# Performance work log

Measured on AMD Instinct MI355X. Metric: run time of the kernel, lower is better.

## Reference

```python
import jax, jax.numpy as jnp
import numpy as np

NUM_HEADS = 16
HEAD_DIM = 64
HIDDEN = NUM_HEADS * HEAD_DIM  # 1024
MAX_POS = 1024


def setup_inputs() -> dict:
    key = jax.random.key(0)
    ks = jax.random.split(key, 6)
    B, L, H = 8, 1024, HIDDEN
    hidden_states = jax.random.normal(ks[0], (B, L, H), dtype=jnp.float32)
    attention_mask = jnp.zeros((B, 1, 1, L), dtype=jnp.float32)
    scale = 0.02  # keep pre-softmax logits in a sane range
    Wq = jax.random.normal(ks[1], (H, H), dtype=jnp.float32) * scale
    Wk = jax.random.normal(ks[2], (H, H), dtype=jnp.float32) * scale
    Wv = jax.random.normal(ks[3], (H, H), dtype=jnp.float32) * scale
    bq = jnp.zeros((H,), dtype=jnp.float32)
    bk = jnp.zeros((H,), dtype=jnp.float32)
    bv = jnp.zeros((H,), dtype=jnp.float32)
    dist_emb = jax.random.normal(ks[4], (2 * MAX_POS - 1, HEAD_DIM), dtype=jnp.float32) * scale
    return {"hidden_states": hidden_states, "attention_mask": attention_mask,
            "Wq": Wq, "bq": bq, "Wk": Wk, "bk": bk, "Wv": Wv, "bv": bv,
            "dist_emb": dist_emb}


def _split_heads(x):
    # [B, L, H] -> [B, nH, L, hd]
    B, L, _ = x.shape
    return x.reshape(B, L, NUM_HEADS, HEAD_DIM).transpose(0, 2, 1, 3)


def reference(hidden_states, attention_mask, Wq, bq, Wk, bk, Wv, bv, dist_emb):
    B, L, H = hidden_states.shape
    q = _split_heads(hidden_states @ Wq.T + bq)  # [B,h,L,d]
    k = _split_heads(hidden_states @ Wk.T + bk)
    v = _split_heads(hidden_states @ Wv.T + bv)

    scores = jnp.einsum("bhld,bhrd->bhlr", q, k)

    # relative_key_query positional bias
    pos_l = jnp.arange(L)[:, None]
    pos_r = jnp.arange(L)[None, :]
    dist_idx = pos_l - pos_r + MAX_POS - 1          # [L, L], in [0, 2*MAX_POS-2]
    pos_emb = dist_emb[dist_idx]                    # [L, L, d]
    scores = scores + jnp.einsum("bhld,lrd->bhlr", q, pos_emb)
    scores = scores + jnp.einsum("bhrd,lrd->bhlr", k, pos_emb)

    scores = scores / jnp.sqrt(jnp.float32(HEAD_DIM))
    scores = scores + attention_mask                # additive mask broadcast [B,1,1,L]
    probs = jax.nn.softmax(scores, axis=-1)         # dropout = identity (eval)
    ctx = jnp.einsum("bhlr,bhrd->bhld", probs, v)
    ctx = ctx.transpose(0, 2, 1, 3).reshape(B, L, H)
    return ctx
```

## Files before the change

### kernel.cpp

```cpp
#include <hip/hip_runtime.h>
#include <stdint.h>

typedef short s16x8 __attribute__((ext_vector_type(8)));
typedef float f32x4 __attribute__((ext_vector_type(4)));

#define MFMA16(a, b, c) __builtin_amdgcn_mfma_f32_16x16x32_bf16((a), (b), (c), 0, 0, 0)

__device__ __forceinline__ ushort f2b(float f) {
  union { float f; uint32_t u; } x; x.f = f;
  uint32_t r = x.u + 0x7fffu + ((x.u >> 16) & 1u);
  return (ushort)(r >> 16);
}
__device__ __forceinline__ float b2f(ushort s) {
  union { uint32_t u; float f; } x; x.u = ((uint32_t)s) << 16;
  return x.f;
}
__device__ __forceinline__ uint32_t pack2t(float a, float b) {
  return __builtin_amdgcn_perm(__float_as_uint(b), __float_as_uint(a), 0x07060302u);
}
__device__ __forceinline__ uint32_t cvtpk(float a, float b) {
  uint32_t r;
  asm("v_cvt_pk_bf16_f32 %0, %1, %2" : "=v"(r) : "v"(a), "v"(b));
  return r;
}

__device__ __forceinline__ void barrier_vm() {
  asm volatile("s_waitcnt vmcnt(0)" ::: "memory");
  __builtin_amdgcn_s_barrier();
}
__device__ __forceinline__ void barrier_lgkm() {
  asm volatile("s_waitcnt lgkmcnt(0)" ::: "memory");
  __builtin_amdgcn_s_barrier();
}

__global__ __launch_bounds__(256) void cast_all(
    const float* __restrict__ hidden, const float* __restrict__ wq,
    const float* __restrict__ wk, const float* __restrict__ wv,
    const float* __restrict__ dist,
    ushort* __restrict__ hb, ushort* __restrict__ wb, ushort* __restrict__ eb) {
  int blk = blockIdx.x;
  const float* src; ushort* dst; int n;
  if (blk < 8192)      { src = hidden; dst = hb; n = 8388608; }
  else if (blk < 9216) { src = wq; dst = wb;               n = 1048576; blk -= 8192; }
  else if (blk < 10240){ src = wk; dst = wb + 1048576;     n = 1048576; blk -= 9216; }
  else if (blk < 11264){ src = wv; dst = wb + 2097152;     n = 1048576; blk -= 10240; }
  else                 { src = dist; dst = eb;             n = 131008;  blk -= 11264; }
  int i = (blk * 256 + threadIdx.x) * 4;
  if (i + 4 <= n) {
    float4 v = *(const float4*)(src + i);
    ushort4 o; o.x = f2b(v.x); o.y = f2b(v.y); o.z = f2b(v.z); o.w = f2b(v.w);
    *(ushort4*)(dst + i) = o;
  }
}

__device__ __forceinline__ void gload16(const void* g, void* l) {
  __builtin_amdgcn_global_load_lds((const __attribute__((address_space(1))) void*)g,
                                   (__attribute__((address_space(3))) void*)l, 16, 0, 0);
}

__global__ __launch_bounds__(256) void qkv_gemm(
    const ushort* __restrict__ hb, const ushort* __restrict__ wb,
    const float* __restrict__ bq, const float* __restrict__ bk, const float* __restrict__ bv,
    ushort* __restrict__ qb, ushort* __restrict__ kb, ushort* __restrict__ vt) {
  __shared__ ushort As[2][4096];
  __shared__ ushort Bs[2][4096];
  const int tid = threadIdx.x;
  const int w = tid >> 6, lane = tid & 63, quad = lane >> 4, l16 = lane & 15;

  const int wg = blockIdx.x;
  const int swz = (wg & 7) * 192 + (wg >> 3);
  const int by = swz / 24;
  const int bx = swz % 24;
  const int m0 = by * 128, n0 = bx * 128;

  const int srow = w * 32 + (lane >> 2);
  const int scol = (lane & 3) * 8;
  const ushort* ga = hb + (size_t)(m0 + srow) * 1024 + scol;
  const ushort* gw = wb + (size_t)(n0 + srow) * 1024 + scol;

  f32x4 acc[4][4];
#pragma unroll
  for (int mt = 0; mt < 4; ++mt)
#pragma unroll
    for (int nt = 0; nt < 4; ++nt) acc[mt][nt] = (f32x4){0.f, 0.f, 0.f, 0.f};

  const int wm = (w >> 1) * 64, wn = (w & 1) * 64;

#define STAGE(C, K0)                                          \
  gload16(ga + (K0), As[C] + w * 1024);                       \
  gload16(ga + (K0) + 16 * 1024, As[C] + w * 1024 + 512);     \
  gload16(gw + (K0), Bs[C] + w * 1024);                       \
  gload16(gw + (K0) + 16 * 1024, Bs[C] + w * 1024 + 512);

#define COMPUTE(C)                                                           \
  {                                                                          \
    s16x8 af[4], bfr[4];                                                     \
    _Pragma("unroll")                                                        \
    for (int mt = 0; mt < 4; ++mt)                                           \
      af[mt] = *(const s16x8*)(As[C] + (wm + 16 * mt + l16) * 32 + quad * 8);\
    _Pragma("unroll")                                                        \
    for (int nt = 0; nt < 4; ++nt)                                           \
      bfr[nt] = *(const s16x8*)(Bs[C] + (wn + 16 * nt + l16) * 32 + quad * 8);\
    _Pragma("unroll")                                                        \
    for (int mt = 0; mt < 4; ++mt)                                           \
      _Pragma("unroll")                                                      \
      for (int nt = 0; nt < 4; ++nt)                                         \
        acc[mt][nt] = MFMA16(af[mt], bfr[nt], acc[mt][nt]);                  \
  }

  STAGE(0, 0)
#pragma unroll 1
  for (int t2 = 0; t2 < 16; ++t2) {
    barrier_vm();
    STAGE(1, t2 * 64 + 32)
    COMPUTE(0)
    barrier_vm();
    if (t2 < 15) { STAGE(0, t2 * 64 + 64) }
    COMPUTE(1)
  }
#undef STAGE
#undef COMPUTE

  const int mat = n0 >> 10;
  const int b = m0 >> 10;
  if (mat < 2) {
    ushort* outp = (mat == 0) ? qb : kb;
    const float* bias = (mat == 0) ? bq : bk;
#pragma unroll
    for (int mt = 0; mt < 4; ++mt) {
      int mbase = m0 + wm + 16 * mt + 4 * quad;
#pragma unroll
      for (int nt = 0; nt < 4; ++nt) {
        int n = n0 + wn + 16 * nt + l16;
        int o = n & 1023; int hh = o >> 6; int d = o & 63;
        float bsv = bias[o];
#pragma unroll
        for (int reg = 0; reg < 4; ++reg) {
          int l = (mbase + reg) & 1023;
          outp[(((size_t)(b * 16 + hh)) * 1024 + l) * 64 + d] = f2b(acc[mt][nt][reg] + bsv);
        }
      }
    }
  } else {
#pragma unroll
    for (int mt = 0; mt < 4; ++mt) {
      int mbase = m0 + wm + 16 * mt + 4 * quad;
      int lb = mbase & 1023;
#pragma unroll
      for (int nt = 0; nt < 4; ++nt) {
        int n = n0 + wn + 16 * nt + l16;
        int o = n & 1023; int hh = o >> 6; int d = o & 63;
        float bsv = bv[o];
        uint2 pk;
        pk.x = cvtpk(acc[mt][nt][0] + bsv, acc[mt][nt][1] + bsv);
        pk.y = cvtpk(acc[mt][nt][2] + bsv, acc[mt][nt][3] + bsv);
        *(uint2*)(vt + (((size_t)(b * 16 + hh)) * 64 + d) * 1024 + lb) = pk;
      }
    }
  }
}

#define KR  0
#define VR  8192
#define ER  16384
#define SER 28672
#define PR  35072

__global__ __launch_bounds__(256, 2) void attn_kernel(
    const ushort* __restrict__ qb, const ushort* __restrict__ kb,
    const ushort* __restrict__ vt, const ushort* __restrict__ eb,
    const float* __restrict__ mask, float* __restrict__ out, int bh0) {
  __shared__ __align__(16) ushort sm[39168];
  const int tid = threadIdx.x;
  const int w = tid >> 6, lane = tid & 63, quad = lane >> 4, l16 = lane & 15;
  const int bh = blockIdx.y + bh0, b = bh >> 4, h = bh & 15;
  const int l0 = blockIdx.x * 64;

  const int srow = lane >> 3;
  const int colb = ((lane & 7) ^ srow) * 8;
  const int row0 = w * 8 + srow;

  const ushort* kp = kb + ((size_t)bh * 1024 + row0) * 64 + colb;
  const ushort* vp = vt + ((size_t)bh * 64 + row0) * 1024 + colb;
  const float* maskp = mask + b * 1024 + l16;

  const int p0 = blockIdx.x % 3;

  {
    const ushort* qp = qb + ((size_t)bh * 1024 + l0 + row0) * 64 + colb;
    gload16(qp,         sm + PR + w * 512);
    gload16(qp + 2048,  sm + PR + 2048 + w * 512);
    gload16(kp,         sm + KR + w * 512);
    gload16(kp + 2048,  sm + KR + 2048 + w * 512);
    gload16(vp,         sm + VR + w * 512);
    gload16(vp + 32768, sm + VR + 2048 + w * 512);
    const int t0i = l0 + 960;
#pragma unroll
    for (int c2 = 0; c2 < 4; ++c2) {
      int jb = w * 8 + 32 * c2;
      int seg = p0 + (jb >> 6); if (seg >= 3) seg -= 3;
      int t = t0i + jb + srow; if (t > 2046) t = 2046;
      gload16(eb + (size_t)t * 64 + colb, sm + ER + seg * 4096 + (jb & 63) * 64);
    }
  }

  const int lm7 = l16 & 7;
  const int swzq = (quad ^ lm7) * 8;
  int offR0[4], offR1[4];
#pragma unroll
  for (int nt = 0; nt < 4; ++nt) {
    offR0[nt] = (16 * nt + l16) * 64 + swzq;
    offR1[nt] = offR0[nt] ^ 32;
  }
  const int offW0 = (w * 16 + l16) * 64 + swzq;
  const int offW1 = offW0 ^ 32;
  const int offPW0 = PR + offW0, offPW1 = PR + offW1;
  const int offWK0 = ((3 - w) * 16 + l16) * 64 + swzq;
  const int offWK1 = offWK0 ^ 32;
  int eoffA[5]; bool selA[5];
#pragma unroll
  for (int i = 0; i < 5; ++i) {
    int ba = w + i;
    eoffA[i] = ((ba & 3) * 16 + l16) * 64 + swzq;  selA[i] = (ba & 4) != 0;
  }
  int offSW[5];
#pragma unroll
  for (int i = 0; i < 5; ++i)
    offSW[i] = SER + (3 - w) * 1600 + (16 * i + l16) * 20 + 4 * quad;
  const int bbF = SER + (w * 16 + 4 * quad + 15 - l16) * 20 + l16;
  int addrP[4][4];
#pragma unroll
  for (int nt = 0; nt < 4; ++nt)
#pragma unroll
    for (int reg = 0; reg < 4; ++reg)
      addrP[nt][reg] = PR + (w * 16 + 4 * quad + reg) * 64
                     + (((2 * nt + (l16 >> 3)) ^ ((4 * quad + reg) & 7)) * 8) + lm7;
  int bidx[4]; bool bcnd[4];
#pragma unroll
  for (int r = 0; r < 4; ++r) {
    bidx[r] = (quad * 16 + ((4 * quad + r + 15 - l16) & 15)) * 4;
    bcnd[r] = (4 * quad + r) > l16;
  }

  barrier_vm();

  const s16x8 aq0 = *(const s16x8*)(sm + offPW0);
  const s16x8 aq1 = *(const s16x8*)(sm + offPW1);

  float rsum[4];
  f32x4 o_acc[4];
#pragma unroll
  for (int r = 0; r < 4; ++r) rsum[r] = 0.f;
#pragma unroll
  for (int nt = 0; nt < 4; ++nt) o_acc[nt] = (f32x4){0.f, 0.f, 0.f, 0.f};
  const f32x4 ZACC = {0.f, 0.f, 0.f, 0.f};

  const float LOG2E = 1.44269504088896f;
  const float SC = 0.125f * LOG2E;

  int s0 = p0;

#define ATTN_ITER(P)                                                               \
  {                                                                                \
    const int it = 2 * ith + (P);                                                  \
    const int r0 = it * 64;                                                        \
    if (it > 0) barrier_vm();     \
          \
    {                                                                              \
      const int rn = (r0 + 64) & 1023;                                             \
      gload16(kp + rn * 64,        sm + KR + 4096 * (1 - (P)) + w * 512);          \
      gload16(kp + rn * 64 + 2048, sm + KR + 4096 * (1 - (P)) + 2048 + w * 512);   \
      gload16(vp + rn,             sm + VR + 4096 * (1 - (P)) + w * 512);          \
      gload16(vp + rn + 32768,     sm + VR + 4096 * (1 - (P)) + 2048 + w * 512);   \
      int pnew = s0 + 2; if (pnew >= 3) pnew -= 3;                                 \
      const int tb = l0 + 960 - r0 - 64;                                           \
      _Pragma("unroll")                                                            \
      for (int c2 = 0; c2 < 2; ++c2) {                                             \
        int o = w * 8 + 32 * c2;                                                   \
        int t = tb + o + srow; t = t < 0 ? 0 : (t > 2046 ? 2046 : t);              \
        gload16(eb + (size_t)t * 64 + colb, sm + ER + pnew * 4096 + o * 64);       \
      }                                                                            \
    }                                                                              \
    float mkv[4];                                                                  \
    _Pragma("unroll")                                                              \
    for (int nt = 0; nt < 4; ++nt) mkv[nt] = maskp[r0 + 16 * nt] * LOG2E;          \
    const int sA4 = s0 * 4096;                                                     \
    int sBi = s0 + 1; if (sBi >= 3) sBi -= 3;                                      \
    const int sB4 = sBi * 4096;                                                    \
    const ushort* KbP = sm + KR + 4096 * (P);                                      \
                                              \
    __builtin_amdgcn_s_setprio(1);                                                 \
    f32x4 zv[4];                                                                   \
    _Pragma("unroll")                                                              \
    for (int nt = 0; nt < 4; ++nt) {                                               \
      s16x8 bk0 = *(const s16x8*)(KbP + offR0[nt]);                                \
      s16x8 bk1 = *(const s16x8*)(KbP + offR1[nt]);                                \
      f32x4 z = MFMA16(aq0, bk0, ZACC);                                            \
      zv[nt] = MFMA16(aq1, bk1, z);                                                \
    }                                                                              \
     \
    const s16x8 ak0 = *(const s16x8*)(KbP + offWK0);                               \
    const s16x8 ak1 = *(const s16x8*)(KbP + offWK1);                               \
    f32x4 d1[5];                                                                   \
    _Pragma("unroll")                                                              \
    for (int i = 0; i < 5; ++i) {                                                  \
      int ea = (selA[i] ? sB4 : sA4) + eoffA[i];                                   \
      s16x8 be0 = *(const s16x8*)(sm + ER + ea);                                   \
      s16x8 be1 = *(const s16x8*)(sm + ER + (ea ^ 32));                            \
      f32x4 z = MFMA16(aq0, be0, ZACC);                                            \
      d1[i] = MFMA16(aq1, be1, z);                                                 \
      f32x4 y = MFMA16(ak0, be0, ZACC);                                            \
      y = MFMA16(ak1, be1, y);                                                     \
      uint2 pk; pk.x = pack2t(y[0], y[1]); pk.y = pack2t(y[2], y[3]);              \
      *(uint2*)(sm + offSW[i]) = pk;                                               \
    }                                                                              \
    __builtin_amdgcn_s_setprio(0);                                                 \
                                  \
    _Pragma("unroll")                                                              \
    for (int r = 0; r < 4; ++r) {                                                  \
      float bp[5];                                                                 \
      _Pragma("unroll")                                                            \
      for (int i = 0; i < 5; ++i)                                                  \
        bp[i] = __int_as_float(                                                    \
            __builtin_amdgcn_ds_bpermute(bidx[r], __float_as_int(d1[i][r])));      \
      _Pragma("unroll")                                                            \
      for (int nt = 0; nt < 4; ++nt)                                               \
        zv[nt][r] += bcnd[r] ? bp[4 - nt] : bp[3 - nt];                            \
    }                                                                              \
    barrier_lgkm();                   \
                    \
    _Pragma("unroll")                                                              \
    for (int nt = 0; nt < 4; ++nt) {                                               \
      _Pragma("unroll")                                                            \
      for (int reg = 0; reg < 4; ++reg) {                                          \
        float z2 = (zv[nt][reg] + b2f(sm[bbF + nt * 1600 + reg * 20])) * SC        \
                 + mkv[nt];                                                        \
        float pe = exp2f(z2);                                                      \
        zv[nt][reg] = pe;                                                          \
        rsum[reg] += pe;                                                           \
      }                                                                            \
    }                                                                              \
               \
    _Pragma("unroll")                                                              \
    for (int nt = 0; nt < 4; ++nt) {                                               \
      uint32_t u01 = cvtpk(zv[nt][0], zv[nt][1]);                                  \
      uint32_t u23 = cvtpk(zv[nt][2], zv[nt][3]);                                  \
      sm[addrP[nt][0]] = (ushort)u01;                                              \
      sm[addrP[nt][1]] = (ushort)(u01 >> 16);                                      \
      sm[addrP[nt][2]] = (ushort)u23;                                              \
      sm[addrP[nt][3]] = (ushort)(u23 >> 16);                                      \
    }                                                                              \
       \
    __builtin_amdgcn_s_setprio(1);                                                 \
    {                                                                              \
      const ushort* VbP = sm + VR + 4096 * (P);                                    \
      const s16x8 ap0 = *(const s16x8*)(sm + offPW0);                              \
      _Pragma("unroll")                                                            \
      for (int nt = 0; nt < 4; ++nt) {                                             \
        s16x8 bv0 = *(const s16x8*)(VbP + offR0[nt]);                              \
        o_acc[nt] = MFMA16(ap0, bv0, o_acc[nt]);                                   \
      }                                                                            \
      const s16x8 ap1 = *(const s16x8*)(sm + offPW1);                              \
      _Pragma("unroll")                                                            \
      for (int nt = 0; nt < 4; ++nt) {                                             \
        s16x8 bv1 = *(const s16x8*)(VbP + offR1[nt]);                              \
        o_acc[nt] = MFMA16(ap1, bv1, o_acc[nt]);                                   \
      }                                                                            \
    }                                                                              \
    __builtin_amdgcn_s_setprio(0);                                                 \
    s0 = (s0 == 0) ? 2 : s0 - 1;                   \
  }

#pragma unroll 1
  for (int ith = 0; ith < 8; ++ith) {
    ATTN_ITER(0)
    ATTN_ITER(1)
  }
#undef ATTN_ITER

#pragma unroll
  for (int off = 1; off < 16; off <<= 1)
#pragma unroll
    for (int reg = 0; reg < 4; ++reg)
      rsum[reg] += __shfl_xor(rsum[reg], off);

#pragma unroll
  for (int nt = 0; nt < 4; ++nt)
#pragma unroll
    for (int reg = 0; reg < 4; ++reg) {
      int l = l0 + w * 16 + 4 * quad + reg;
      int d = 16 * nt + l16;
      out[((size_t)(b * 1024 + l)) * 1024 + h * 64 + d] = o_acc[nt][reg] / rsum[reg];
    }
}

extern "C" void kernel_launch(void* const* d_in, const int* in_sizes, int n_in,
                              void* d_out, int out_size, void* d_ws, size_t ws_size,
                              hipStream_t stream) {
  const float* hidden = (const float*)d_in[0];
  const float* mask   = (const float*)d_in[1];
  const float* Wq     = (const float*)d_in[2];
  const float* bq     = (const float*)d_in[3];
  const float* Wk     = (const float*)d_in[4];
  const float* bk     = (const float*)d_in[5];
  const float* Wv     = (const float*)d_in[6];
  const float* bv     = (const float*)d_in[7];
  const float* dist   = (const float*)d_in[8];
  float* out = (float*)d_out;

  ushort* ws = (ushort*)d_ws;
  ushort* qb = ws;
  ushort* kb = ws + 8388608;
  ushort* vt = ws + 16777216;
  ushort* hb = ws + 25165824;
  ushort* wb = ws + 33554432;
  ushort* eb = ws + 36700160;

  cast_all<<<11392, 256, 0, stream>>>(hidden, Wq, Wk, Wv, dist, hb, wb, eb);
  qkv_gemm<<<1536, 256, 0, stream>>>(hb, wb, bq, bk, bv, qb, kb, vt);
  attn_kernel<<<dim3(16, 64), 256, 0, stream>>>(qb, kb, vt, eb, mask, out, 0);
  attn_kernel<<<dim3(16, 64), 256, 0, stream>>>(qb, kb, vt, eb, mask, out, 64);
}
```

Measured before the change: 372.1 us.

## Enlarge QKV GEMM tile to 256x128 and merge attention launches

The QKV projection GEMM now computes 256x128 output tiles per block, with each wave handling 128 rows in two halves that reuse the same B fragments. The grid is halved and the swizzle adjusted, and the barrier now also waits on LDS counters. The two half-size attention launches are merged into one 128-head-batch launch to cut launch overhead and tail effects. The larger tile doubles the accumulator registers and A-tile LDS, which may reduce occupancy despite the launch-bounds hint of 3.

```diff
diff --git a/kernel.cpp b/kernel.cpp
--- a/kernel.cpp
+++ b/kernel.cpp
@@ -26,6 +26,10 @@
 
 __device__ __forceinline__ void barrier_vm() {
   asm volatile("s_waitcnt vmcnt(0)" ::: "memory");
+  __builtin_amdgcn_s_barrier();
+}
+__device__ __forceinline__ void barrier_vm_lgkm() {
+  asm volatile("s_waitcnt vmcnt(0) lgkmcnt(0)" ::: "memory");
   __builtin_amdgcn_s_barrier();
 }
 __device__ __forceinline__ void barrier_lgkm() {
@@ -58,63 +62,70 @@
                                    (__attribute__((address_space(3))) void*)l, 16, 0, 0);
 }
 
-__global__ __launch_bounds__(256) void qkv_gemm(
+__global__ __launch_bounds__(256, 3) void qkv_gemm(
     const ushort* __restrict__ hb, const ushort* __restrict__ wb,
     const float* __restrict__ bq, const float* __restrict__ bk, const float* __restrict__ bv,
     ushort* __restrict__ qb, ushort* __restrict__ kb, ushort* __restrict__ vt) {
-  __shared__ ushort As[2][4096];
+  __shared__ ushort As[2][8192];
   __shared__ ushort Bs[2][4096];
   const int tid = threadIdx.x;
   const int w = tid >> 6, lane = tid & 63, quad = lane >> 4, l16 = lane & 15;
 
   const int wg = blockIdx.x;
-  const int swz = (wg & 7) * 192 + (wg >> 3);
+  const int swz = (wg & 7) * 96 + (wg >> 3);
   const int by = swz / 24;
   const int bx = swz % 24;
-  const int m0 = by * 128, n0 = bx * 128;
-
-  const int srow = w * 32 + (lane >> 2);
-  const int scol = (lane & 3) * 8;
-  const ushort* ga = hb + (size_t)(m0 + srow) * 1024 + scol;
-  const ushort* gw = wb + (size_t)(n0 + srow) * 1024 + scol;
-
-  f32x4 acc[4][4];
-#pragma unroll
-  for (int mt = 0; mt < 4; ++mt)
+  const int m0 = by * 256, n0 = bx * 128;
+
+  const int arow = lane >> 2;
+  const int acol = (lane & 3) * 8;
+  const ushort* ga = hb + (size_t)(m0 + arow) * 1024 + acol;
+  const ushort* gw = wb + (size_t)(n0 + arow) * 1024 + acol;
+
+  f32x4 acc[8][4];
+#pragma unroll
+  for (int mt = 0; mt < 8; ++mt)
 #pragma unroll
     for (int nt = 0; nt < 4; ++nt) acc[mt][nt] = (f32x4){0.f, 0.f, 0.f, 0.f};
 
-  const int wm = (w >> 1) * 64, wn = (w & 1) * 64;
-
-#define STAGE(C, K0)                                          \
-  gload16(ga + (K0), As[C] + w * 1024);                       \
-  gload16(ga + (K0) + 16 * 1024, As[C] + w * 1024 + 512);     \
-  gload16(gw + (K0), Bs[C] + w * 1024);                       \
-  gload16(gw + (K0) + 16 * 1024, Bs[C] + w * 1024 + 512);
-
-#define COMPUTE(C)                                                           \
-  {                                                                          \
-    s16x8 af[4], bfr[4];                                                     \
-    _Pragma("unroll")                                                        \
-    for (int mt = 0; mt < 4; ++mt)                                           \
-      af[mt] = *(const s16x8*)(As[C] + (wm + 16 * mt + l16) * 32 + quad * 8);\
-    _Pragma("unroll")                                                        \
-    for (int nt = 0; nt < 4; ++nt)                                           \
+  const int wm = (w >> 1) * 128, wn = (w & 1) * 64;
+
+#define STAGE(C, K0)                                                      \
+  gload16(ga + (K0) + (size_t)((w)      * 16) * 1024, As[C] + (w)      * 512); \
+  gload16(ga + (K0) + (size_t)((w + 4)  * 16) * 1024, As[C] + (w + 4)  * 512); \
+  gload16(ga + (K0) + (size_t)((w + 8)  * 16) * 1024, As[C] + (w + 8)  * 512); \
+  gload16(ga + (K0) + (size_t)((w + 12) * 16) * 1024, As[C] + (w + 12) * 512); \
+  gload16(gw + (K0) + (size_t)((w)      * 16) * 1024, Bs[C] + (w)      * 512); \
+  gload16(gw + (K0) + (size_t)((w + 4)  * 16) * 1024, Bs[C] + (w + 4)  * 512);
+
+#define COMPUTE(C)                                                            \
+  {                                                                           \
+    s16x8 bfr[4];                                                             \
+    _Pragma("unroll")                                                         \
+    for (int nt = 0; nt < 4; ++nt)                                            \
       bfr[nt] = *(const s16x8*)(Bs[C] + (wn + 16 * nt + l16) * 32 + quad * 8);\
-    _Pragma("unroll")                                                        \
-    for (int mt = 0; mt < 4; ++mt)                                           \
-      _Pragma("unroll")                                                      \
-      for (int nt = 0; nt < 4; ++nt)                                         \
-        acc[mt][nt] = MFMA16(af[mt], bfr[nt], acc[mt][nt]);                  \
+    _Pragma("unroll")                                                         \
+    for (int half = 0; half < 2; ++half) {                                    \
+      s16x8 af[4];                                                            \
+      _Pragma("unroll")                                                       \
+      for (int mt = 0; mt < 4; ++mt)                                          \
+        af[mt] = *(const s16x8*)(As[C] +                                      \
+                    (wm + 64 * half + 16 * mt + l16) * 32 + quad * 8);        \
+      _Pragma("unroll")                                                       \
+      for (int mt = 0; mt < 4; ++mt)                                          \
+        _Pragma("unroll")                                                     \
+        for (int nt = 0; nt < 4; ++nt)                                        \
+          acc[half * 4 + mt][nt] = MFMA16(af[mt], bfr[nt], acc[half * 4 + mt][nt]); \
+    }                                                                         \
   }
 
   STAGE(0, 0)
 #pragma unroll 1
   for (int t2 = 0; t2 < 16; ++t2) {
-    barrier_vm();
+    barrier_vm_lgkm();
     STAGE(1, t2 * 64 + 32)
     COMPUTE(0)
-    barrier_vm();
+    barrier_vm_lgkm();
     if (t2 < 15) { STAGE(0, t2 * 64 + 64) }
     COMPUTE(1)
   }
@@ -127,7 +138,7 @@
     ushort* outp = (mat == 0) ? qb : kb;
     const float* bias = (mat == 0) ? bq : bk;
 #pragma unroll
-    for (int mt = 0; mt < 4; ++mt) {
+    for (int mt = 0; mt < 8; ++mt) {
       int mbase = m0 + wm + 16 * mt + 4 * quad;
 #pragma unroll
       for (int nt = 0; nt < 4; ++nt) {
@@ -143,7 +154,7 @@
     }
   } else {
 #pragma unroll
-    for (int mt = 0; mt < 4; ++mt) {
+    for (int mt = 0; mt < 8; ++mt) {
       int mbase = m0 + wm + 16 * mt + 4 * quad;
       int lb = mbase & 1023;
 #pragma unroll
@@ -169,11 +180,11 @@
 __global__ __launch_bounds__(256, 2) void attn_kernel(
     const ushort* __restrict__ qb, const ushort* __restrict__ kb,
     const ushort* __restrict__ vt, const ushort* __restrict__ eb,
-    const float* __restrict__ mask, float* __restrict__ out, int bh0) {
+    const float* __restrict__ mask, float* __restrict__ out) {
   __shared__ __align__(16) ushort sm[39168];
   const int tid = threadIdx.x;
   const int w = tid >> 6, lane = tid & 63, quad = lane >> 4, l16 = lane & 15;
-  const int bh = blockIdx.y + bh0, b = bh >> 4, h = bh & 15;
+  const int bh = blockIdx.y, b = bh >> 4, h = bh & 15;
   const int l0 = blockIdx.x * 64;
 
   const int srow = lane >> 3;
@@ -417,7 +428,6 @@
   ushort* eb = ws + 36700160;
 
   cast_all<<<11392, 256, 0, stream>>>(hidden, Wq, Wk, Wv, dist, hb, wb, eb);
-  qkv_gemm<<<1536, 256, 0, stream>>>(hb, wb, bq, bk, bv, qb, kb, vt);
-  attn_kernel<<<dim3(16, 64), 256, 0, stream>>>(qb, kb, vt, eb, mask, out, 0);
-  attn_kernel<<<dim3(16, 64), 256, 0, stream>>>(qb, kb, vt, eb, mask, out, 64);
-}
+  qkv_gemm<<<768, 256, 0, stream>>>(hb, wb, bq, bk, bv, qb, kb, vt);
+  attn_kernel<<<dim3(16, 128), 256, 0, stream>>>(qb, kb, vt, eb, mask, out);
+}
```

Result: faster. 340.1 us (-8.6%).
